# Kernel tuning notes

Hardware: AMD Instinct MI355X
Metric: run time of the kernel (lower is better)

## Reference

```python
import jax, jax.numpy as jnp
import numpy as np
from jax import lax

K = 5  # nearest neighbors (includes self)
EPS = 1e-6


def _relu(a):
    return jnp.maximum(a, 0.0)


def setup_inputs() -> dict:
    key = jax.random.key(0)
    ks = jax.random.split(key, 16)
    B, N, D = 8, 4096, 2
    LD = 64  # local_dim

    def w(k, fan_in, fan_out):
        return jax.random.normal(k, (fan_in, fan_out), jnp.float32) / np.sqrt(fan_in)

    x = jax.random.normal(ks[0], (B, N, D), jnp.float32)
    inp = {
        "x": x,
        # local_mlp: D->64->128->LD
        "lw1": w(ks[1], D, 64), "lb1": jnp.zeros((64,), jnp.float32),
        "lw2": w(ks[2], 64, 128), "lb2": jnp.zeros((128,), jnp.float32),
        "lw3": w(ks[3], 128, LD), "lb3": jnp.zeros((LD,), jnp.float32),
        # cls_branch: (D+LD)->128->128
        "cw1": w(ks[4], D + LD, 128), "cb1": jnp.zeros((128,), jnp.float32),
        "cw2": w(ks[5], 128, 128), "cb2": jnp.zeros((128,), jnp.float32),
        # topo_branch: LD->128->128
        "tw1": w(ks[6], LD, 128), "tb1": jnp.zeros((128,), jnp.float32),
        "tw2": w(ks[7], 128, 128), "tb2": jnp.zeros((128,), jnp.float32),
    }
    return inp


def reference(x, lw1, lb1, lw2, lb2, lw3, lb3,
              cw1, cb1, cw2, cb2, tw1, tb1, tw2, tb2):
    B, N, D = x.shape
    # squared pairwise distances (B,N,N)
    sq = jnp.sum(x * x, axis=-1)
    dist_sq = sq[:, :, None] + sq[:, None, :] - 2.0 * jnp.einsum("bnd,bmd->bnm", x, x)
    _, idx = lax.top_k(-dist_sq, K)  # (B,N,K) nearest (self first)

    neighbors = x[jnp.arange(B)[:, None, None], idx]          # (B,N,K,D)
    rel = neighbors - x[:, :, None, :]                         # relative coords
    centered = rel - rel.mean(axis=2, keepdims=True)           # (B,N,K,D)
    cov = jnp.einsum("bnki,bnkj->bnij", centered, centered) / (K - 1)

    e, v = jnp.linalg.eigh(cov + EPS * jnp.eye(2, dtype=x.dtype))  # ascending eigvals
    v1 = v[..., :, 1]                                          # principal eigenvector
    base_angle = jnp.arctan2(v1[..., 1], v1[..., 0])[..., None]  # (B,N,1)

    base_axes = jnp.sqrt(jnp.maximum(e, EPS))                  # (B,N,2)
    base_axes = base_axes[..., ::-1]                           # descending: major first
    base_axes = base_axes / (base_axes.max(axis=-1, keepdims=True) + EPS)
    base_axes = jnp.maximum(base_axes, 0.2)

    lcc = jnp.einsum("bnki,bnij->bnkj", centered, v)           # canonical coords
    h = _relu(lcc @ lw1 + lb1)
    h = _relu(h @ lw2 + lb2)
    h = _relu(h @ lw3 + lb3)                                   # (B,N,K,LD)
    local_feats = h.max(axis=2)                                # (B,N,LD)

    cls_in = jnp.concatenate([x, local_feats], axis=-1)
    cls_features = _relu(_relu(cls_in @ cw1 + cb1) @ cw2 + cb2)
    topo_features = _relu(_relu(local_feats @ tw1 + tb1) @ tw2 + tb2)
    return (cls_features, topo_features, base_angle, base_axes)
```

## Files before the change

### kernel.cpp

```cpp
#include <hip/hip_runtime.h>
#include <math.h>

#pragma clang fp contract(off)

#define NPTS 4096
#define PTS  32768
#define ROWS 163840
#define QN   8
#define QLEN 512
#define SLOTS 8

#define EPS_L   5.9604644775390625e-8f
#define EPS2_L  3.5527136788005009e-15f
#define SAFMIN_L 1.1754943508222875e-38f

__device__ __forceinline__ float frn_mul(float a, float b) { float r = a * b; return r; }
__device__ __forceinline__ float frn_add(float a, float b) { float r = a + b; return r; }
__device__ __forceinline__ float frn_sub(float a, float b) { float r = a - b; return r; }
__device__ __forceinline__ float frn_div(float a, float b) { float r = a / b; return r; }

__device__ __forceinline__ float ref_sq(float x0, float x1) {
  return frn_add(frn_mul(x0, x0), frn_mul(x1, x1));
}
__device__ __forceinline__ float ref_key(float nx, float ny, float sqn,
                                         float mx, float my, float sqm) {
  float dot = fmaf(ny, my, frn_mul(nx, mx));
  float s = frn_add(sqn, sqm);
  return fmaf(-2.0f, dot, s);
}

__global__ __launch_bounds__(256) void prep_w(
    const float* __restrict__ lw1, const float* __restrict__ lw2, const float* __restrict__ lw3,
    const float* __restrict__ cw1, const float* __restrict__ cw2,
    const float* __restrict__ tw1, const float* __restrict__ tw2,
    float* __restrict__ wt) {
  const int Ks[7]   = {2, 64, 128, 66, 128, 64, 128};
  const int Kp[7]   = {2, 64, 128, 80, 128, 64, 128};
  const int Ns[7]   = {64, 128, 64, 128, 128, 128, 128};
  const int offs[7] = {0, 128, 8320, 16512, 26752, 43136, 51328};
  const float* srcs[7] = {lw1, lw2, lw3, cw1, cw2, tw1, tw2};
  int b = blockIdx.x;
  const float* src = srcs[b];
  float* dst = wt + offs[b];
  int K = Ks[b], KP = Kp[b], N = Ns[b];
  for (int e = threadIdx.x; e < KP * N; e += 256) {
    int j = e / KP, i = e - j * KP;
    dst[e] = (i < K) ? src[i * N + j] : 0.0f;
  }
}

__device__ __forceinline__ void cand_step(float mex, float mey, float cx, float cy,
                                          unsigned int idx, unsigned int T,
                                          unsigned int* sbuf, int t,
                                          unsigned int& cnt) {
  float dx = mex - cx, dy = mey - cy;
  float dist = fmaf(dy, dy, dx * dx);
  unsigned int v = (__float_as_uint(dist) & 0xFFFFF000u) | idx;
  sbuf[cnt * 256 + t] = v;
  cnt += (v < T) ? 1u : 0u;
}

__global__ __launch_bounds__(256) void knn_scan(const float* __restrict__ x,
                                                unsigned int* __restrict__ ipart) {
  __shared__ float2 cand[QLEN];
  __shared__ unsigned int sbuf[16 * 256];
  int bx = blockIdx.x;
  int q = bx & (QN - 1);
  int pg = bx >> 3;
  int batch = pg >> 4;
  const float* xb = x + (size_t)batch * NPTS * 2;
  int c0 = q * QLEN;
  for (int i = threadIdx.x; i < QLEN; i += 256)
    cand[i] = ((const float2*)xb)[c0 + i];
  __syncthreads();
  int t = threadIdx.x;
  int p = pg * 256 + t;
  float2 me = ((const float2*)x)[p];
  unsigned int d[SLOTS];
#pragma unroll
  for (int s = 0; s < SLOTS; s++) d[s] = 0xFFFFFFFFu;
  unsigned int T = 0xFFFFFFFFu;
  unsigned int cnt = 0;
  for (int mm = 0; mm < QLEN / 4; mm++) {
    float4 c01 = ((const float4*)cand)[2 * mm];
    float4 c23 = ((const float4*)cand)[2 * mm + 1];
    unsigned int idx0 = (unsigned int)(c0 + 4 * mm);
    cand_step(me.x, me.y, c01.x, c01.y, idx0 + 0u, T, sbuf, t, cnt);
    cand_step(me.x, me.y, c01.z, c01.w, idx0 + 1u, T, sbuf, t, cnt);
    cand_step(me.x, me.y, c23.x, c23.y, idx0 + 2u, T, sbuf, t, cnt);
    cand_step(me.x, me.y, c23.z, c23.w, idx0 + 3u, T, sbuf, t, cnt);
    if (__any((int)(cnt >= 13u))) {
#pragma unroll
      for (int j = 0; j < 16; j++) {
        unsigned int u = ((unsigned)j < cnt) ? sbuf[j * 256 + t] : 0xFFFFFFFFu;
#pragma unroll
        for (int s = 0; s < SLOTS; s++) {
          unsigned int lo = min(u, d[s]);
          unsigned int hi = max(u, d[s]);
          d[s] = lo; u = hi;
        }
      }
      cnt = 0;
      T = d[SLOTS - 1];
    }
  }
#pragma unroll
  for (int j = 0; j < 16; j++) {
    unsigned int u = ((unsigned)j < cnt) ? sbuf[j * 256 + t] : 0xFFFFFFFFu;
#pragma unroll
    for (int s = 0; s < SLOTS; s++) {
      unsigned int lo = min(u, d[s]);
      unsigned int hi = max(u, d[s]);
      d[s] = lo; u = hi;
    }
  }
#pragma unroll
  for (int s = 0; s < SLOTS; s++)
    ipart[((size_t)(q * SLOTS + s)) * PTS + p] = d[s];
}

__global__ __launch_bounds__(128) void merge_geom(const float* __restrict__ x,
    const unsigned int* __restrict__ ipart,
    float2* __restrict__ lcct2,
    float* __restrict__ angle_out, float2* __restrict__ axes_out,
    float* __restrict__ lftx) {
  int p = blockIdx.x * 128 + threadIdx.x;
  int batch = p >> 12;
  const float2* xb = (const float2*)(x + (size_t)batch * NPTS * 2);
  float2 me = ((const float2*)x)[p];
  lftx[p] = me.x;
  lftx[PTS + p] = me.y;
#pragma unroll
  for (int r = 66; r < 80; r++) lftx[(size_t)r * PTS + p] = 0.0f;
  float sqn = ref_sq(me.x, me.y);

  unsigned int g[SLOTS];
#pragma unroll
  for (int s = 0; s < SLOTS; s++) g[s] = 0xFFFFFFFFu;
  for (int qs = 0; qs < QN * SLOTS; qs++) {
    unsigned int v = ipart[(size_t)qs * PTS + p];
#pragma unroll
    for (int s = 0; s < SLOTS; s++) {
      unsigned int lo = min(v, g[s]);
      unsigned int hi = max(v, g[s]);
      g[s] = lo; v = hi;
    }
  }
  float dk[5]; int id[5];
#pragma unroll
  for (int s = 0; s < 5; s++) { dk[s] = 3.0e38f; id[s] = 0x7fffffff; }
#pragma unroll
  for (int s8 = 0; s8 < SLOTS; s8++) {
    int ci = (int)(g[s8] & 0xFFFu);
    float2 c = xb[ci];
    float key = ref_key(me.x, me.y, sqn, c.x, c.y, ref_sq(c.x, c.y));
    float v = key; int vi = ci;
#pragma unroll
    for (int s = 0; s < 5; s++) {
      bool lt = (v < dk[s]) || (v == dk[s] && vi < id[s]);
      float tv = dk[s]; int ti = id[s];
      if (lt) { dk[s] = v; id[s] = vi; v = tv; vi = ti; }
    }
  }
  float rx[5], ry[5];
  float sx = 0.f, sy = 0.f;
#pragma unroll
  for (int k = 0; k < 5; k++) {
    float2 nb = xb[id[k]];
    rx[k] = frn_sub(nb.x, me.x); ry[k] = frn_sub(nb.y, me.y);
    sx = frn_add(sx, rx[k]); sy = frn_add(sy, ry[k]);
  }
  float mx = frn_div(sx, 5.0f), my = frn_div(sy, 5.0f);
  float c00 = 0.f, c01 = 0.f, c11 = 0.f;
#pragma unroll
  for (int k = 0; k < 5; k++) {
    rx[k] = frn_sub(rx[k], mx); ry[k] = frn_sub(ry[k], my);
    c00 = frn_add(c00, frn_mul(rx[k], rx[k]));
    c01 = frn_add(c01, frn_mul(rx[k], ry[k]));
    c11 = frn_add(c11, frn_mul(ry[k], ry[k]));
  }
  c00 = frn_div(c00, 4.0f); c01 = frn_div(c01, 4.0f); c11 = frn_div(c11, 4.0f);
  float A = frn_add(c00, 1e-6f), Bv = c01, C = frn_add(c11, 1e-6f);

  float absA = fabsf(A), absC = fabsf(C), absB = fabsf(Bv);
  float thr = frn_mul(frn_mul(sqrtf(absA), sqrtf(absC)), EPS_L);
  bool diag = (absB == 0.f) || (absB <= thr);
  if (!diag) {
    bool qr = (absC < absA);
    float b2 = frn_mul(absB, absB);
    float t = qr ? frn_add(frn_mul(frn_mul(EPS2_L, absC), absA), SAFMIN_L)
                 : frn_add(frn_mul(frn_mul(EPS2_L, absA), absC), SAFMIN_L);
    if (b2 <= t) diag = true;
  }
  float e1, e2, v00, v10, v01, v11;
  if (diag) {
    if (C < A) { e1 = C; e2 = A; v00 = 0.f; v10 = 1.f; v01 = 1.f; v11 = 0.f; }
    else       { e1 = A; e2 = C; v00 = 1.f; v10 = 0.f; v01 = 0.f; v11 = 1.f; }
  } else {
    float sm = frn_add(A, C), df = frn_sub(A, C);
    float adf = fabsf(df), tb = frn_add(Bv, Bv), ab = fabsf(tb);
    float rt;
    if (adf > ab) {
      float r = frn_div(ab, adf);
      rt = frn_mul(adf, sqrtf(frn_add(1.0f, frn_mul(r, r))));
    } else if (adf < ab) {
      float r = frn_div(adf, ab);
      rt = frn_mul(ab, sqrtf(frn_add(1.0f, frn_mul(r, r))));
    } else {
      rt = frn_mul(ab, sqrtf(2.0f));
    }
    float acmx, acmn;
    if (absA > absC) { acmx = A; acmn = C; } else { acmx = C; acmn = A; }
    float rt1, rt2; int sgn1;
    if (sm < 0.f) {
      rt1 = frn_mul(0.5f, frn_sub(sm, rt)); sgn1 = -1;
      rt2 = frn_sub(frn_mul(frn_div(acmx, rt1), acmn), frn_mul(frn_div(Bv, rt1), Bv));
    } else if (sm > 0.f) {
      rt1 = frn_mul(0.5f, frn_add(sm, rt)); sgn1 = 1;
      rt2 = frn_sub(frn_mul(frn_div(acmx, rt1), acmn), frn_mul(frn_div(Bv, rt1), Bv));
    } else {
      rt1 = frn_mul(0.5f, rt); rt2 = frn_mul(-0.5f, rt); sgn1 = 1;
    }
    float cs, cs1, sn1; int sgn2;
    if (df >= 0.f) { cs = frn_add(df, rt); sgn2 = 1; }
    else           { cs = frn_sub(df, rt); sgn2 = -1; }
    float acs = fabsf(cs);
    if (acs > ab) {
      float ct = frn_div(-tb, cs);
      sn1 = frn_div(1.0f, sqrtf(frn_add(1.0f, frn_mul(ct, ct))));
      cs1 = frn_mul(ct, sn1);
    } else {
      if (ab == 0.f) { cs1 = 1.0f; sn1 = 0.0f; }
      else {
        float tn = frn_div(-cs, tb);
        cs1 = frn_div(1.0f, sqrtf(frn_add(1.0f, frn_mul(tn, tn))));
        sn1 = frn_mul(tn, cs1);
      }
    }
    if (sgn1 == sgn2) { float t = cs1; cs1 = -sn1; sn1 = t; }
    if (rt2 < rt1) { e1 = rt2; e2 = rt1; v00 = -sn1; v10 = cs1; v01 = cs1;  v11 = sn1; }
    else           { e1 = rt1; e2 = rt2; v00 = cs1;  v10 = sn1; v01 = -sn1; v11 = cs1; }
  }

  angle_out[p] = atan2f(v11, v01);
  float aM = sqrtf(fmaxf(e2, 1e-6f));
  float am = sqrtf(fmaxf(e1, 1e-6f));
  float den = frn_add(fmaxf(aM, am), 1e-6f);
  axes_out[p] = make_float2(fmaxf(frn_div(aM, den), 0.2f),
                            fmaxf(frn_div(am, den), 0.2f));

  size_t rowb = (size_t)p * 5;
#pragma unroll
  for (int k = 0; k < 5; k++) {
    float l0 = frn_add(frn_mul(rx[k], v00), frn_mul(ry[k], v10));
    float l1 = frn_add(frn_mul(rx[k], v01), frn_mul(ry[k], v11));
    lcct2[rowb + k] = make_float2(l0, l1);
  }
}

__global__ __launch_bounds__(256, 3) void gemm_l2(
    const float2* __restrict__ lcct2, const float* __restrict__ lw1t,
    const float* __restrict__ lb1,
    const float* __restrict__ wt, const float* __restrict__ bias,
    float* __restrict__ out_t, int M) {
  __shared__ float alds[16 * 128];
  __shared__ float wlds[16 * 128];
  __shared__ float w1s[192];
  int t = threadIdx.x;
  int m0 = blockIdx.x * 128;
  if (t < 192) w1s[t] = (t < 128) ? lw1t[t] : lb1[t - 128];
  int mloc = t & 127;
  int kbase = t >> 7;
  float2 lme = lcct2[m0 + mloc];
  int tm = t & 15;
  int tn = t >> 4;
  float acc[8][8];
#pragma unroll
  for (int j = 0; j < 8; j++) {
    float b = bias[tn * 8 + j];
#pragma unroll
    for (int i = 0; i < 8; i++) acc[j][i] = b;
  }
  for (int kt = 0; kt < 4; kt++) {
    int k0 = kt * 16;
    __syncthreads();
#pragma unroll
    for (int pp = 0; pp < 8; pp++) {
      int kk = pp * 2 + kbase;
      int k = k0 + kk;
      float h = fmaf(lme.y, w1s[2 * k + 1], fmaf(lme.x, w1s[2 * k], w1s[128 + k]));
      alds[kk * 128 + mloc] = fmaxf(h, 0.f);
    }
#pragma unroll
    for (int pp = 0; pp < 2; pp++) {
      int e = pp * 256 + t;
      int n = e >> 2;
      int kc = e & 3;
      float4 v = *(const float4*)(wt + (size_t)n * 64 + k0 + kc * 4);
      wlds[(kc * 4 + 0) * 128 + n] = v.x;
      wlds[(kc * 4 + 1) * 128 + n] = v.y;
      wlds[(kc * 4 + 2) * 128 + n] = v.z;
      wlds[(kc * 4 + 3) * 128 + n] = v.w;
    }
    __syncthreads();
#pragma unroll
    for (int kk = 0; kk < 16; kk++) {
      float af[8], wf[8];
      *(float4*)(af)     = *(const float4*)(alds + kk * 128 + tm * 8);
      *(float4*)(af + 4) = *(const float4*)(alds + kk * 128 + tm * 8 + 4);
      *(float4*)(wf)     = *(const float4*)(wlds + kk * 128 + tn * 8);
      *(float4*)(wf + 4) = *(const float4*)(wlds + kk * 128 + tn * 8 + 4);
#pragma unroll
      for (int j = 0; j < 8; j++)
#pragma unroll
        for (int i = 0; i < 8; i++)
          acc[j][i] = fmaf(af[i], wf[j], acc[j][i]);
    }
  }
#pragma unroll
  for (int j = 0; j < 8; j++) {
    int n = tn * 8 + j;
    float4 o0, o1;
    o0.x = fmaxf(acc[j][0], 0.f); o0.y = fmaxf(acc[j][1], 0.f);
    o0.z = fmaxf(acc[j][2], 0.f); o0.w = fmaxf(acc[j][3], 0.f);
    o1.x = fmaxf(acc[j][4], 0.f); o1.y = fmaxf(acc[j][5], 0.f);
    o1.z = fmaxf(acc[j][6], 0.f); o1.w = fmaxf(acc[j][7], 0.f);
    float* dst = out_t + (size_t)n * M + m0 + tm * 8;
    *(float4*)(dst) = o0;
    *(float4*)(dst + 4) = o1;
  }
}

__global__ __launch_bounds__(512, 4) void gemm_l3max(
    const float* __restrict__ h2, const float* __restrict__ wt,
    const float* __restrict__ bias, float* __restrict__ lftx) {
  __shared__ float alds[16 * 320];
  __shared__ float wlds[16 * 64];
  int t = threadIdx.x;
  int m0 = blockIdx.x * 320;
  int pt = t & 63;
  int ng = t >> 6;
  float acc[5][8];
#pragma unroll
  for (int j = 0; j < 8; j++) {
    float b = bias[ng * 8 + j];
#pragma unroll
    for (int r = 0; r < 5; r++) acc[r][j] = b;
  }
  for (int kt = 0; kt < 8; kt++) {
    int k0 = kt * 16;
    __syncthreads();
    for (int e = t; e < 1280; e += 512) {
      int kk = e / 80;
      int m4 = e - kk * 80;
      float4 v = *(const float4*)(h2 + (size_t)(k0 + kk) * ROWS + m0 + m4 * 4);
      *(float4*)(alds + kk * 320 + m4 * 4) = v;
    }
    if (t < 256) {
      int n = t >> 2, kc = t & 3;
      float4 v = *(const float4*)(wt + (size_t)n * 128 + k0 + kc * 4);
      wlds[(kc * 4 + 0) * 64 + n] = v.x;
      wlds[(kc * 4 + 1) * 64 + n] = v.y;
      wlds[(kc * 4 + 2) * 64 + n] = v.z;
      wlds[(kc * 4 + 3) * 64 + n] = v.w;
    }
    __syncthreads();
#pragma unroll
    for (int kk = 0; kk < 16; kk++) {
      float af[5], wf[8];
#pragma unroll
      for (int r = 0; r < 5; r++) af[r] = alds[kk * 320 + pt * 5 + r];
      *(float4*)(wf)     = *(const float4*)(wlds + kk * 64 + ng * 8);
      *(float4*)(wf + 4) = *(const float4*)(wlds + kk * 64 + ng * 8 + 4);
#pragma unroll
      for (int r = 0; r < 5; r++)
#pragma unroll
        for (int j = 0; j < 8; j++)
          acc[r][j] = fmaf(af[r], wf[j], acc[r][j]);
    }
  }
  int p = blockIdx.x * 64 + pt;
#pragma unroll
  for (int j = 0; j < 8; j++) {
    float r0 = fmaxf(acc[0][j], 0.f), r1 = fmaxf(acc[1][j], 0.f);
    float r2 = fmaxf(acc[2][j], 0.f), r3 = fmaxf(acc[3][j], 0.f);
    float r4 = fmaxf(acc[4][j], 0.f);
    float m = fmaxf(fmaxf(fmaxf(r0, r1), fmaxf(r2, r3)), r4);
    lftx[(size_t)(ng * 8 + j + 2) * PTS + p] = m;
  }
}

__global__ __launch_bounds__(256, 3) void gemm_head1(
    const float* __restrict__ lftx, const float* __restrict__ wtbase,
    const float* __restrict__ cb1, const float* __restrict__ tb1,
    float* __restrict__ a1c, float* __restrict__ a1t) {
  __shared__ float alds[16 * 128];
  __shared__ float wlds[16 * 128];
  int bid = blockIdx.x;
  bool isC = bid < 256;
  const float* in_t = isC ? lftx : (lftx + 2 * PTS);
  const float* wt   = isC ? (wtbase + 16512) : (wtbase + 43136);
  const float* bias = isC ? cb1 : tb1;
  float* out_t      = isC ? a1c : a1t;
  int Kstr = isC ? 80 : 64;
  int KT   = isC ? 5 : 4;
  int m0 = (bid & 255) * 128;
  int t = threadIdx.x;
  int tm = t & 15;
  int tn = t >> 4;
  float acc[8][8];
#pragma unroll
  for (int j = 0; j < 8; j++) {
    float b = bias[tn * 8 + j];
#pragma unroll
    for (int i = 0; i < 8; i++) acc[j][i] = b;
  }
  for (int kt = 0; kt < KT; kt++) {
    int k0 = kt * 16;
    __syncthreads();
#pragma unroll
    for (int pp = 0; pp < 2; pp++) {
      int e = pp * 256 + t;
      int kk = e >> 5;
      int m4 = e & 31;
      float4 v = *(const float4*)(in_t + (size_t)(k0 + kk) * PTS + m0 + m4 * 4);
      *(float4*)(alds + kk * 128 + m4 * 4) = v;
    }
#pragma unroll
    for (int pp = 0; pp < 2; pp++) {
      int e = pp * 256 + t;
      int n = e >> 2;
      int kc = e & 3;
      float4 v = *(const float4*)(wt + (size_t)n * Kstr + k0 + kc * 4);
      wlds[(kc * 4 + 0) * 128 + n] = v.x;
      wlds[(kc * 4 + 1) * 128 + n] = v.y;
      wlds[(kc * 4 + 2) * 128 + n] = v.z;
      wlds[(kc * 4 + 3) * 128 + n] = v.w;
    }
    __syncthreads();
#pragma unroll
    for (int kk = 0; kk < 16; kk++) {
      float af[8], wf[8];
      *(float4*)(af)     = *(const float4*)(alds + kk * 128 + tm * 8);
      *(float4*)(af + 4) = *(const float4*)(alds + kk * 128 + tm * 8 + 4);
      *(float4*)(wf)     = *(const float4*)(wlds + kk * 128 + tn * 8);
      *(float4*)(wf + 4) = *(const float4*)(wlds + kk * 128 + tn * 8 + 4);
#pragma unroll
      for (int j = 0; j < 8; j++)
#pragma unroll
        for (int i = 0; i < 8; i++)
          acc[j][i] = fmaf(af[i], wf[j], acc[j][i]);
    }
  }
#pragma unroll
  for (int j = 0; j < 8; j++) {
    int n = tn * 8 + j;
    float4 o0, o1;
    o0.x = fmaxf(acc[j][0], 0.f); o0.y = fmaxf(acc[j][1], 0.f);
    o0.z = fmaxf(acc[j][2], 0.f); o0.w = fmaxf(acc[j][3], 0.f);
    o1.x = fmaxf(acc[j][4], 0.f); o1.y = fmaxf(acc[j][5], 0.f);
    o1.z = fmaxf(acc[j][6], 0.f); o1.w = fmaxf(acc[j][7], 0.f);
    float* dst = out_t + (size_t)n * PTS + m0 + tm * 8;
    *(float4*)(dst) = o0;
    *(float4*)(dst + 4) = o1;
  }
}

__global__ __launch_bounds__(256, 3) void gemm_head2(
    const float* __restrict__ a1c, const float* __restrict__ a1t,
    const float* __restrict__ wtbase,
    const float* __restrict__ cb2, const float* __restrict__ tb2,
    float* __restrict__ outbase) {
  __shared__ float alds[16 * 128];
  __shared__ float wlds[16 * 128];
  int bid = blockIdx.x;
  bool isC = bid < 256;
  const float* in_t = isC ? a1c : a1t;
  const float* wt   = isC ? (wtbase + 26752) : (wtbase + 51328);
  const float* bias = isC ? cb2 : tb2;
  float* out        = isC ? outbase : (outbase + 4194304);
  int m0 = (bid & 255) * 128;
  int t = threadIdx.x;
  int tm = t & 15;
  int tn = t >> 4;
  float acc[8][8];
#pragma unroll
  for (int j = 0; j < 8; j++) {
    float b = bias[tn * 8 + j];
#pragma unroll
    for (int i = 0; i < 8; i++) acc[j][i] = b;
  }
  for (int kt = 0; kt < 8; kt++) {
    int k0 = kt * 16;
    __syncthreads();
#pragma unroll
    for (int pp = 0; pp < 2; pp++) {
      int e = pp * 256 + t;
      int kk = e >> 5;
      int m4 = e & 31;
      float4 v = *(const float4*)(in_t + (size_t)(k0 + kk) * PTS + m0 + m4 * 4);
      *(float4*)(alds + kk * 128 + m4 * 4) = v;
    }
#pragma unroll
    for (int pp = 0; pp < 2; pp++) {
      int e = pp * 256 + t;
      int n = e >> 2;
      int kc = e & 3;
      float4 v = *(const float4*)(wt + (size_t)n * 128 + k0 + kc * 4);
      wlds[(kc * 4 + 0) * 128 + n] = v.x;
      wlds[(kc * 4 + 1) * 128 + n] = v.y;
      wlds[(kc * 4 + 2) * 128 + n] = v.z;
      wlds[(kc * 4 + 3) * 128 + n] = v.w;
    }
    __syncthreads();
#pragma unroll
    for (int kk = 0; kk < 16; kk++) {
      float af[8], wf[8];
      *(float4*)(af)     = *(const float4*)(alds + kk * 128 + tm * 8);
      *(float4*)(af + 4) = *(const float4*)(alds + kk * 128 + tm * 8 + 4);
      *(float4*)(wf)     = *(const float4*)(wlds + kk * 128 + tn * 8);
      *(float4*)(wf + 4) = *(const float4*)(wlds + kk * 128 + tn * 8 + 4);
#pragma unroll
      for (int j = 0; j < 8; j++)
#pragma unroll
        for (int i = 0; i < 8; i++)
          acc[j][i] = fmaf(af[i], wf[j], acc[j][i]);
    }
  }
#pragma unroll
  for (int i = 0; i < 8; i++) {
    int m = m0 + tm * 8 + i;
    float4 o0, o1;
    o0.x = fmaxf(acc[0][i], 0.f); o0.y = fmaxf(acc[1][i], 0.f);
    o0.z = fmaxf(acc[2][i], 0.f); o0.w = fmaxf(acc[3][i], 0.f);
    o1.x = fmaxf(acc[4][i], 0.f); o1.y = fmaxf(acc[5][i], 0.f);
    o1.z = fmaxf(acc[6][i], 0.f); o1.w = fmaxf(acc[7][i], 0.f);
    float* dst = out + (size_t)m * 128 + tn * 8;
    *(float4*)(dst) = o0;
    *(float4*)(dst + 4) = o1;
  }
}

extern "C" void kernel_launch(void* const* d_in, const int* in_sizes, int n_in,
                              void* d_out, int out_size, void* d_ws, size_t ws_size,
                              hipStream_t stream) {
  const float* x   = (const float*)d_in[0];
  const float* lb1 = (const float*)d_in[2];
  const float* lb2 = (const float*)d_in[4];
  const float* lb3 = (const float*)d_in[6];
  const float* cb1 = (const float*)d_in[8];
  const float* cb2 = (const float*)d_in[10];
  const float* tb1 = (const float*)d_in[12];
  const float* tb2 = (const float*)d_in[14];

  float* out = (float*)d_out;
  float* angle_out = out + 8388608;
  float* axes_out  = out + 8421376;

  float* W = (float*)d_ws;
  float* wt    = W;
  float* R1    = W + 67712;
  float* R2    = R1 + 10485760;
  float* R3    = R2 + 10485760;
  float* lftx  = R3 + 20971520;
  float* lcct2 = lftx + 2621440;
  unsigned int* ipart = (unsigned int*)R1;
  float* a1c   = R2;
  float* a1t   = R2 + 4194304;
  float* h2    = R3;

  prep_w<<<7, 256, 0, stream>>>((const float*)d_in[1], (const float*)d_in[3], (const float*)d_in[5],
                                (const float*)d_in[7], (const float*)d_in[9],
                                (const float*)d_in[11], (const float*)d_in[13], wt);
  knn_scan<<<1024, 256, 0, stream>>>(x, ipart);
  merge_geom<<<256, 128, 0, stream>>>(x, ipart, (float2*)lcct2, angle_out, (float2*)axes_out, lftx);

  gemm_l2<<<ROWS / 128, 256, 0, stream>>>((const float2*)lcct2, wt + 0, lb1,
                                          wt + 128, lb2, h2, ROWS);
  gemm_l3max<<<PTS / 64, 512, 0, stream>>>(h2, wt + 8320, lb3, lftx);

  gemm_head1<<<512, 256, 0, stream>>>(lftx, wt, cb1, tb1, a1c, a1t);
  gemm_head2<<<512, 256, 0, stream>>>(a1c, a1t, wt, cb2, tb2, out);
}
```

Baseline: 306.1 us.

## Replace brute-force kNN scan with uniform grid spatial hashing

```diff
diff --git a/kernel.cpp b/kernel.cpp
--- a/kernel.cpp
+++ b/kernel.cpp
@@ -6,9 +6,13 @@
 #define NPTS 4096
 #define PTS  32768
 #define ROWS 163840
-#define QN   8
-#define QLEN 512
 #define SLOTS 8
+
+#define GRID  32
+#define NCELL (GRID * GRID)
+#define GL    5.0f
+#define GSC   3.2f
+#define CW    0.3125f
 
 #define EPS_L   5.9604644775390625e-8f
 #define EPS2_L  3.5527136788005009e-15f
@@ -27,6 +31,11 @@
   float dot = fmaf(ny, my, frn_mul(nx, mx));
   float s = frn_add(sqn, sqm);
   return fmaf(-2.0f, dot, s);
+}
+
+__device__ __forceinline__ int cell_of(float v) {
+  int c = (int)floorf((v + GL) * GSC);
+  return min(max(c, 0), GRID - 1);
 }
 
 __global__ __launch_bounds__(256) void prep_w(
@@ -49,74 +58,101 @@
   }
 }
 
-__device__ __forceinline__ void cand_step(float mex, float mey, float cx, float cy,
-                                          unsigned int idx, unsigned int T,
-                                          unsigned int* sbuf, int t,
-                                          unsigned int& cnt) {
-  float dx = mex - cx, dy = mey - cy;
-  float dist = fmaf(dy, dy, dx * dx);
-  unsigned int v = (__float_as_uint(dist) & 0xFFFFF000u) | idx;
-  sbuf[cnt * 256 + t] = v;
-  cnt += (v < T) ? 1u : 0u;
-}
-
-__global__ __launch_bounds__(256) void knn_scan(const float* __restrict__ x,
-                                                unsigned int* __restrict__ ipart) {
-  __shared__ float2 cand[QLEN];
-  __shared__ unsigned int sbuf[16 * 256];
-  int bx = blockIdx.x;
-  int q = bx & (QN - 1);
-  int pg = bx >> 3;
-  int batch = pg >> 4;
-  const float* xb = x + (size_t)batch * NPTS * 2;
-  int c0 = q * QLEN;
-  for (int i = threadIdx.x; i < QLEN; i += 256)
-    cand[i] = ((const float2*)xb)[c0 + i];
+__global__ __launch_bounds__(128) void grid_hist(const float* __restrict__ x,
+                                                 unsigned int* __restrict__ hist) {
+  int p = blockIdx.x * 128 + threadIdx.x;
+  float2 me = ((const float2*)x)[p];
+  int b = p >> 12;
+  int cx = cell_of(me.x), cy = cell_of(me.y);
+  atomicAdd(&hist[b * NCELL + cy * GRID + cx], 1u);
+}
+
+__global__ __launch_bounds__(1024) void grid_scan(const unsigned int* __restrict__ hist,
+                                                  unsigned int* __restrict__ base,
+                                                  unsigned int* __restrict__ cursor) {
+  __shared__ unsigned int sh[NCELL];
+  int b = blockIdx.x, t = threadIdx.x;
+  unsigned int v = hist[b * NCELL + t];
+  sh[t] = v;
   __syncthreads();
-  int t = threadIdx.x;
-  int p = pg * 256 + t;
+  for (int off = 1; off < NCELL; off <<= 1) {
+    unsigned int u = (t >= off) ? sh[t - off] : 0u;
+    __syncthreads();
+    sh[t] += u;
+    __syncthreads();
+  }
+  unsigned int g = (unsigned int)(b * NPTS) + sh[t] - v;
+  base[b * NCELL + t] = g;
+  cursor[b * NCELL + t] = g;
+}
+
+__global__ __launch_bounds__(128) void grid_scatter(const float* __restrict__ x,
+                                                    unsigned int* __restrict__ cursor,
+                                                    float2* __restrict__ sxy,
+                                                    unsigned int* __restrict__ sid) {
+  int p = blockIdx.x * 128 + threadIdx.x;
   float2 me = ((const float2*)x)[p];
+  int b = p >> 12;
+  int cx = cell_of(me.x), cy = cell_of(me.y);
+  unsigned int slot = atomicAdd(&cursor[b * NCELL + cy * GRID + cx], 1u);
+  sxy[slot] = me;
+  sid[slot] = (unsigned int)(p & (NPTS - 1));
+}
+
+#define VISIT_CELL(cx, cy) do {                                        \
+    int _cell = (cy) * GRID + (cx);                                    \
+    unsigned int _st = cb[_cell];                                      \
+    unsigned int _en = _st + ch[_cell];                                \
+    for (unsigned int _i = _st; _i < _en; _i++) {                      \
+      float2 _c = sxy[_i];                                             \
+      unsigned int _ci = sid[_i];                                      \
+      float _dx = me.x - _c.x, _dy = me.y - _c.y;                      \
+      float _dist = fmaf(_dy, _dy, _dx * _dx);                         \
+      unsigned int _v = (__float_as_uint(_dist) & 0xFFFFF000u) | _ci;  \
+      _Pragma("unroll")                                                \
+      for (int _k = 0; _k < SLOTS; _k++) {                             \
+        unsigned int _lo = min(_v, d[_k]);                             \
+        unsigned int _hi = max(_v, d[_k]);                             \
+        d[_k] = _lo; _v = _hi;                                         \
+      }                                                                \
+    }                                                                  \
+  } while (0)
+
+__global__ __launch_bounds__(128) void grid_query(
+    const float2* __restrict__ sxy, const unsigned int* __restrict__ sid,
+    const unsigned int* __restrict__ base, const unsigned int* __restrict__ hist,
+    unsigned int* __restrict__ ipart) {
+  int s = blockIdx.x * 128 + threadIdx.x;
+  int b = s >> 12;
+  float2 me = sxy[s];
+  int myloc = (int)sid[s];
+  int hx = cell_of(me.x), hy = cell_of(me.y);
+  const unsigned int* cb = base + b * NCELL;
+  const unsigned int* ch = hist + b * NCELL;
   unsigned int d[SLOTS];
 #pragma unroll
-  for (int s = 0; s < SLOTS; s++) d[s] = 0xFFFFFFFFu;
-  unsigned int T = 0xFFFFFFFFu;
-  unsigned int cnt = 0;
-  for (int mm = 0; mm < QLEN / 4; mm++) {
-    float4 c01 = ((const float4*)cand)[2 * mm];
-    float4 c23 = ((const float4*)cand)[2 * mm + 1];
-    unsigned int idx0 = (unsigned int)(c0 + 4 * mm);
-    cand_step(me.x, me.y, c01.x, c01.y, idx0 + 0u, T, sbuf, t, cnt);
-    cand_step(me.x, me.y, c01.z, c01.w, idx0 + 1u, T, sbuf, t, cnt);
-    cand_step(me.x, me.y, c23.x, c23.y, idx0 + 2u, T, sbuf, t, cnt);
-    cand_step(me.x, me.y, c23.z, c23.w, idx0 + 3u, T, sbuf, t, cnt);
-    if (__any((int)(cnt >= 13u))) {
-#pragma unroll
-      for (int j = 0; j < 16; j++) {
-        unsigned int u = ((unsigned)j < cnt) ? sbuf[j * 256 + t] : 0xFFFFFFFFu;
-#pragma unroll
-        for (int s = 0; s < SLOTS; s++) {
-          unsigned int lo = min(u, d[s]);
-          unsigned int hi = max(u, d[s]);
-          d[s] = lo; u = hi;
-        }
+  for (int k = 0; k < SLOTS; k++) d[k] = 0xFFFFFFFFu;
+  for (int r = 0; r < GRID; r++) {
+    if (r >= 2) {
+      float lb = (float)(r - 1) * CW;
+      float lbsq = lb * lb * 0.999f;
+      unsigned int vb = __float_as_uint(lbsq) & 0xFFFFF000u;
+      if (vb > d[SLOTS - 1]) break;
+    }
+    int x0 = max(hx - r, 0), x1 = min(hx + r, GRID - 1);
+    int y0 = max(hy - r, 0), y1 = min(hy + r, GRID - 1);
+    for (int cy = y0; cy <= y1; cy++) {
+      if (cy == hy - r || cy == hy + r) {
+        for (int cx = x0; cx <= x1; cx++) VISIT_CELL(cx, cy);
+      } else {
+        if (hx - r >= 0)        VISIT_CELL(hx - r, cy);
+        if (hx + r <= GRID - 1) VISIT_CELL(hx + r, cy);
       }
-      cnt = 0;
-      T = d[SLOTS - 1];
-    }
-  }
-#pragma unroll
-  for (int j = 0; j < 16; j++) {
-    unsigned int u = ((unsigned)j < cnt) ? sbuf[j * 256 + t] : 0xFFFFFFFFu;
-#pragma unroll
-    for (int s = 0; s < SLOTS; s++) {
-      unsigned int lo = min(u, d[s]);
-      unsigned int hi = max(u, d[s]);
-      d[s] = lo; u = hi;
-    }
-  }
-#pragma unroll
-  for (int s = 0; s < SLOTS; s++)
-    ipart[((size_t)(q * SLOTS + s)) * PTS + p] = d[s];
+    }
+  }
+  int gp = b * NPTS + myloc;
+#pragma unroll
+  for (int k = 0; k < SLOTS; k++) ipart[(size_t)k * PTS + gp] = d[k];
 }
 
 __global__ __launch_bounds__(128) void merge_geom(const float* __restrict__ x,
@@ -136,16 +172,8 @@
 
   unsigned int g[SLOTS];
 #pragma unroll
-  for (int s = 0; s < SLOTS; s++) g[s] = 0xFFFFFFFFu;
-  for (int qs = 0; qs < QN * SLOTS; qs++) {
-    unsigned int v = ipart[(size_t)qs * PTS + p];
-#pragma unroll
-    for (int s = 0; s < SLOTS; s++) {
-      unsigned int lo = min(v, g[s]);
-      unsigned int hi = max(v, g[s]);
-      g[s] = lo; v = hi;
-    }
-  }
+  for (int s = 0; s < SLOTS; s++) g[s] = ipart[(size_t)s * PTS + p];
+
   float dk[5]; int id[5];
 #pragma unroll
   for (int s = 0; s < 5; s++) { dk[s] = 3.0e38f; id[s] = 0x7fffffff; }
@@ -564,15 +592,25 @@
   float* R3    = R2 + 10485760;
   float* lftx  = R3 + 20971520;
   float* lcct2 = lftx + 2621440;
-  unsigned int* ipart = (unsigned int*)R1;
+  float* gbuf  = lcct2 + 327680;
+  unsigned int* ipart  = (unsigned int*)R1;
   float* a1c   = R2;
   float* a1t   = R2 + 4194304;
   float* h2    = R3;
+  unsigned int* hist   = (unsigned int*)gbuf;
+  unsigned int* gbase  = hist + 8 * NCELL;
+  unsigned int* cursor = gbase + 8 * NCELL;
+  unsigned int* sid    = cursor + 8 * NCELL;
+  float2* sxy          = (float2*)(sid + PTS);
 
   prep_w<<<7, 256, 0, stream>>>((const float*)d_in[1], (const float*)d_in[3], (const float*)d_in[5],
                                 (const float*)d_in[7], (const float*)d_in[9],
                                 (const float*)d_in[11], (const float*)d_in[13], wt);
-  knn_scan<<<1024, 256, 0, stream>>>(x, ipart);
+  hipMemsetAsync(hist, 0, 8 * NCELL * sizeof(unsigned int), stream);
+  grid_hist<<<PTS / 128, 128, 0, stream>>>(x, hist);
+  grid_scan<<<8, NCELL, 0, stream>>>(hist, gbase, cursor);
+  grid_scatter<<<PTS / 128, 128, 0, stream>>>(x, cursor, sxy, sid);
+  grid_query<<<PTS / 128, 128, 0, stream>>>(sxy, sid, gbase, hist, ipart);
   merge_geom<<<256, 128, 0, stream>>>(x, ipart, (float2*)lcct2, angle_out, (float2*)axes_out, lftx);
 
   gemm_l2<<<ROWS / 128, 256, 0, stream>>>((const float2*)lcct2, wt + 0, lb1,
```

New measurement: 351.3 us. +14.8%, slower.
